# Kernel tuning notes

Measured on AMD Instinct MI355X. Metric: run time of the kernel, lower is better.

Reference implementation:

```python
import jax, jax.numpy as jnp
import numpy as np

B, S, D = 1, 2048, 4096
H, KVH, HD = 32, 8, 128


def setup_inputs() -> dict:
    key = jax.random.key(0)
    ks = jax.random.split(key, 6)
    x = jax.random.normal(ks[0], (B, S, D), dtype=jnp.float32)
    # Llama3 RoPE angles: theta = 500000
    inv_freq = 1.0 / (500000.0 ** (np.arange(0, HD, 2, dtype=np.float32) / HD))
    ang = np.arange(S, dtype=np.float32)[:, None] * inv_freq[None, :]  # [S, HD//2]
    freqs_cos = jnp.asarray(np.cos(ang), dtype=jnp.float32)
    freqs_sin = jnp.asarray(np.sin(ang), dtype=jnp.float32)
    sc = 0.02
    wq = jax.random.normal(ks[1], (H * HD, D), dtype=jnp.float32) * sc
    wk = jax.random.normal(ks[2], (KVH * HD, D), dtype=jnp.float32) * sc
    wv = jax.random.normal(ks[3], (KVH * HD, D), dtype=jnp.float32) * sc
    wo = jax.random.normal(ks[4], (D, H * HD), dtype=jnp.float32) * sc
    return {"x": x, "freqs_cos": freqs_cos, "freqs_sin": freqs_sin,
            "wq": wq, "wk": wk, "wv": wv, "wo": wo}


def _rope(t, cos, sin):
    # t: [B, S, h, HD]; rotate consecutive pairs (complex multiply)
    t2 = t.reshape(*t.shape[:-1], HD // 2, 2)
    x0, x1 = t2[..., 0], t2[..., 1]
    c = cos[None, :, None, :]
    s = sin[None, :, None, :]
    r0 = x0 * c - x1 * s
    r1 = x0 * s + x1 * c
    return jnp.stack([r0, r1], axis=-1).reshape(t.shape)


def reference(x, freqs_cos, freqs_sin, wq, wk, wv, wo):
    b, s, _ = x.shape
    q = jnp.einsum('bsd,ed->bse', x, wq).reshape(b, s, H, HD)
    k = jnp.einsum('bsd,ed->bse', x, wk).reshape(b, s, KVH, HD)
    v = jnp.einsum('bsd,ed->bse', x, wv).reshape(b, s, KVH, HD)
    q = _rope(q, freqs_cos, freqs_sin)
    k = _rope(k, freqs_cos, freqs_sin)
    # GQA: repeat kv heads
    rep = H // KVH
    k = jnp.repeat(k, rep, axis=2)
    v = jnp.repeat(v, rep, axis=2)
    scale = 1.0 / jnp.sqrt(jnp.asarray(HD, dtype=x.dtype))
    scores = jnp.einsum('bqhd,bkhd->bhqk', q, k) * scale
    causal = jnp.tril(jnp.ones((s, s), dtype=bool))
    scores = jnp.where(causal[None, None], scores, jnp.finfo(scores.dtype).min)
    p = jax.nn.softmax(scores, axis=-1)
    out = jnp.einsum('bhqk,bkhd->bqhd', p, v).reshape(b, s, H * HD)
    return jnp.einsum('bse,de->bsd', out, wo)
```

## Files before the change

kernel.cpp:

```cpp
#include <hip/hip_runtime.h>

typedef unsigned short u16;
typedef short bf16x8 __attribute__((ext_vector_type(8)));
typedef float f32x4 __attribute__((ext_vector_type(4)));

#define S_LEN 2048
#define ATT_SCALE (0.08838834764831845f * 1.4426950408889634f)
#define NEG_BIG  -1.0e30f

static __device__ __forceinline__ float bf2f(u16 u) {
  union { unsigned int i; float f; } v; v.i = ((unsigned int)u) << 16; return v.f;
}
static __device__ __forceinline__ u16 f2bf(float f) {
  union { float f; unsigned int i; } v; v.f = f;
  unsigned int x = v.i;
  return (u16)((x + 0x7fffu + ((x >> 16) & 1u)) >> 16);
}
static __device__ __forceinline__ float fexp2(float x) {
  return __builtin_amdgcn_exp2f(x);
}

static __device__ __forceinline__ void gl_lds16(const u16* g, u16* l) {
  __builtin_amdgcn_global_load_lds(
      (const __attribute__((address_space(1))) unsigned int*)g,
      (__attribute__((address_space(3))) unsigned int*)l, 16, 0, 0);
}

static __device__ __forceinline__ bf16x8 load8(const u16* p) { return *(const bf16x8*)p; }
static __device__ __forceinline__ bf16x8 load8(const float* p) {
  f32x4 a = *(const f32x4*)p;
  f32x4 b = *(const f32x4*)(p + 4);
  bf16x8 r;
  r[0] = (short)f2bf(a[0]); r[1] = (short)f2bf(a[1]);
  r[2] = (short)f2bf(a[2]); r[3] = (short)f2bf(a[3]);
  r[4] = (short)f2bf(b[0]); r[5] = (short)f2bf(b[1]);
  r[6] = (short)f2bf(b[2]); r[7] = (short)f2bf(b[3]);
  return r;
}
static __device__ __forceinline__ void store_out(u16* C, size_t i, float v)  { C[i] = f2bf(v); }
static __device__ __forceinline__ void store_out(float* C, size_t i, float v){ C[i] = v; }

__global__ __launch_bounds__(256) void f2b_kernel(
    const float* __restrict__ s, u16* __restrict__ d, int n8) {
  int i = blockIdx.x * 256 + threadIdx.x;
  if (i >= n8) return;
  *(bf16x8*)&d[(size_t)i * 8] = load8(s + (size_t)i * 8);
}

template <typename OT>
static __device__ __forceinline__ void gemm_core(
    const u16* __restrict__ A, const u16* __restrict__ B, OT* __restrict__ C,
    int K, int ldc, int bm, int bn) {
  __shared__ __align__(16) u16 As[128 * 64];
  __shared__ __align__(16) u16 Bs[128 * 64];
  const int tid  = threadIdx.x;
  const int lane = tid & 63;
  const int wave = tid >> 6;
  const int wm = (wave >> 1) << 6;
  const int wn = (wave & 1) << 6;
  const int col  = lane & 15;
  const int quad = lane >> 4;

  const f32x4 fzero = {0.f, 0.f, 0.f, 0.f};
  f32x4 acc[4][4];
#pragma unroll
  for (int i = 0; i < 4; ++i)
#pragma unroll
    for (int j = 0; j < 4; ++j) acc[i][j] = fzero;

  const int srow = (lane >> 3);
  const int sc8  = lane & 7;

  for (int k0 = 0; k0 < K; k0 += 64) {
#pragma unroll
    for (int i = 0; i < 4; ++i) {
      int r = wave * 32 + i * 8 + srow;
      int src = (sc8 ^ (r & 7)) << 3;
      gl_lds16(A + (size_t)(bm + r) * K + k0 + src, &As[(wave * 32 + i * 8) * 64]);
      gl_lds16(B + (size_t)(bn + r) * K + k0 + src, &Bs[(wave * 32 + i * 8) * 64]);
    }
    __syncthreads();
#pragma unroll
    for (int kk = 0; kk < 64; kk += 32) {
      bf16x8 af[4], bfr[4];
#pragma unroll
      for (int mt = 0; mt < 4; ++mt) {
        int row = wm + mt * 16 + col;
        af[mt] = *(const bf16x8*)&As[row * 64 + ((((kk >> 3) + quad) ^ (col & 7)) << 3)];
      }
#pragma unroll
      for (int nt = 0; nt < 4; ++nt) {
        int row = wn + nt * 16 + col;
        bfr[nt] = *(const bf16x8*)&Bs[row * 64 + ((((kk >> 3) + quad) ^ (col & 7)) << 3)];
      }
#pragma unroll
      for (int mt = 0; mt < 4; ++mt)
#pragma unroll
        for (int nt = 0; nt < 4; ++nt)
          acc[mt][nt] = __builtin_amdgcn_mfma_f32_16x16x32_bf16(
              af[mt], bfr[nt], acc[mt][nt], 0, 0, 0);
    }
    __syncthreads();
  }
#pragma unroll
  for (int mt = 0; mt < 4; ++mt)
#pragma unroll
    for (int nt = 0; nt < 4; ++nt)
#pragma unroll
      for (int r = 0; r < 4; ++r) {
        int row = bm + wm + mt * 16 + quad * 4 + r;
        int cn  = bn + wn + nt * 16 + col;
        store_out(C, (size_t)row * ldc + cn, acc[mt][nt][r]);
      }
}

__global__ __launch_bounds__(256) void gemm_qkv(
    const u16* __restrict__ xb, const u16* __restrict__ wqb,
    const u16* __restrict__ wkb, const u16* __restrict__ wvb,
    u16* __restrict__ q, u16* __restrict__ k, u16* __restrict__ v) {
  int bx = blockIdx.x;
  const u16* B; u16* C; int ldc, bn;
  if (bx < 32)      { B = wqb; C = q; ldc = 4096; bn = bx * 128; }
  else if (bx < 40) { B = wkb; C = k; ldc = 1024; bn = (bx - 32) * 128; }
  else              { B = wvb; C = v; ldc = 1024; bn = (bx - 40) * 128; }
  gemm_core<u16>(xb, B, C, 4096, ldc, blockIdx.y * 128, bn);
}

__global__ __launch_bounds__(256) void gemm_o(
    const u16* __restrict__ ao, const u16* __restrict__ wob, float* __restrict__ out) {
  gemm_core<float>(ao, wob, out, 4096, 4096, blockIdx.y * 128, blockIdx.x * 128);
}

#define LDK 72
template <typename AT, typename BT, typename OT>
__global__ __launch_bounds__(256) void gemm_bt(
    const AT* __restrict__ A, const BT* __restrict__ B,
    OT* __restrict__ C, int M, int N, int K) {
  __shared__ __align__(16) u16 As[128 * LDK];
  __shared__ __align__(16) u16 Bs[128 * LDK];
  const int tid  = threadIdx.x;
  const int lane = tid & 63;
  const int wave = tid >> 6;
  const int wm = (wave >> 1) << 6;
  const int wn = (wave & 1) << 6;
  const int col  = lane & 15;
  const int quad = lane >> 4;
  const int bm = blockIdx.y * 128;
  const int bn = blockIdx.x * 128;

  const f32x4 fzero = {0.f, 0.f, 0.f, 0.f};
  f32x4 acc[4][4];
#pragma unroll
  for (int i = 0; i < 4; ++i)
#pragma unroll
    for (int j = 0; j < 4; ++j) acc[i][j] = fzero;

  const int sr = tid >> 3;
  const int sc = (tid & 7) * 8;
  const AT* Aptr = A + (size_t)(bm + sr) * K + sc;
  const BT* Bptr = B + (size_t)(bn + sr) * K + sc;

  for (int k0 = 0; k0 < K; k0 += 64) {
#pragma unroll
    for (int p = 0; p < 4; ++p) {
      *(bf16x8*)&As[(sr + 32 * p) * LDK + sc] = load8(Aptr + (size_t)(32 * p) * K + k0);
      *(bf16x8*)&Bs[(sr + 32 * p) * LDK + sc] = load8(Bptr + (size_t)(32 * p) * K + k0);
    }
    __syncthreads();
#pragma unroll
    for (int kk = 0; kk < 64; kk += 32) {
      bf16x8 af[4], bfr[4];
#pragma unroll
      for (int mt = 0; mt < 4; ++mt)
        af[mt] = *(const bf16x8*)&As[(wm + mt * 16 + col) * LDK + kk + quad * 8];
#pragma unroll
      for (int nt = 0; nt < 4; ++nt)
        bfr[nt] = *(const bf16x8*)&Bs[(wn + nt * 16 + col) * LDK + kk + quad * 8];
#pragma unroll
      for (int mt = 0; mt < 4; ++mt)
#pragma unroll
        for (int nt = 0; nt < 4; ++nt)
          acc[mt][nt] = __builtin_amdgcn_mfma_f32_16x16x32_bf16(
              af[mt], bfr[nt], acc[mt][nt], 0, 0, 0);
    }
    __syncthreads();
  }
#pragma unroll
  for (int mt = 0; mt < 4; ++mt)
#pragma unroll
    for (int nt = 0; nt < 4; ++nt)
#pragma unroll
      for (int r = 0; r < 4; ++r) {
        int row = bm + wm + mt * 16 + quad * 4 + r;
        int cn  = bn + wn + nt * 16 + col;
        store_out(C, (size_t)row * N + cn, acc[mt][nt][r]);
      }
}

__global__ __launch_bounds__(256) void rope_kernel(
    u16* __restrict__ q, u16* __restrict__ k,
    const float* __restrict__ cs, const float* __restrict__ sn) {
  int idx = blockIdx.x * 256 + threadIdx.x;
  const int QP = S_LEN * 32 * 64;
  u16* base;
  int s, i;
  bool isq = idx < QP;
  if (isq) {
    s = idx >> 11; int w = idx & 2047; i = w & 63;
    base = q + (size_t)s * 4096 + (w >> 6) * 128 + 2 * i;
  } else {
    int j = idx - QP;
    s = j >> 9; int w = j & 511; i = w & 63;
    base = k + (size_t)s * 1024 + (w >> 6) * 128 + 2 * i;
  }
  float c  = cs[s * 64 + i];
  float sv = sn[s * 64 + i];
  float x0 = bf2f(base[0]);
  float x1 = bf2f(base[1]);
  float r0 = x0 * c - x1 * sv;
  float r1 = x0 * sv + x1 * c;
  if (isq) { r0 *= ATT_SCALE; r1 *= ATT_SCALE; }
  base[0] = f2bf(r0);
  base[1] = f2bf(r1);
}

__global__ __launch_bounds__(512, 2) void attn_kernel(
    const u16* __restrict__ Q, const u16* __restrict__ K,
    const u16* __restrict__ V, u16* __restrict__ O) {
  const int ib   = blockIdx.x;
  const int h    = blockIdx.y;
  const int kvh  = h >> 2;
  const int tid  = threadIdx.x;
  const int lane = tid & 63;
  const int wave = tid >> 6;
  const int grp  = wave >> 2;
  const int wl   = wave & 3;
  const int col  = lane & 15;
  const int quad = lane >> 4;
  const int chd  = col >> 3;
  const int gt   = tid & 255;

  __shared__ __align__(16) u16 SMEM[2][16384];
  __shared__ float MLS[256];
  u16* Kb = &SMEM[grp][0];
  u16* Vb = &SMEM[grp][8192];

  const f32x4 fzero = {0.f, 0.f, 0.f, 0.f};

  const int krow = lane >> 4;
  const int kcnk = lane & 15;
  const int vsc  = (gt & 15) * 8;
  const int vrp  = gt >> 4;
  const int vrot = gt & 7;

  for (int t = 0; t < 2; ++t) {
    const int qb = t ? 15 - ib : ib;
    const int rb = qb * 128 + wl * 32;

    bf16x8 qf[2][4];
#pragma unroll
    for (int u = 0; u < 2; ++u)
#pragma unroll
      for (int kb = 0; kb < 4; ++kb)
        qf[u][kb] = *(const bf16x8*)&Q[(size_t)(rb + u * 16 + col) * 4096 +
                                       h * 128 + kb * 32 + quad * 8];

    f32x4 oacc[2][8];
#pragma unroll
    for (int u = 0; u < 2; ++u)
#pragma unroll
      for (int nt = 0; nt < 8; ++nt) oacc[u][nt] = fzero;
    float m_[2] = {NEG_BIG, NEG_BIG};
    float l_[2] = {0.f, 0.f};

    const int nr = qb + 1;
    for (int rnd = 0; rnd < nr; ++rnd) {
      const int c    = grp * nr + rnd;
      const int pos0 = c * 64;

#pragma unroll
      for (int i = 0; i < 4; ++i) {
        int r  = wl * 16 + i * 4 + krow;
        int g  = (kcnk & 8) |
                 ((((kcnk ^ r) & 7) + (((r >> 3) & 1) << 2)) & 7);
        gl_lds16(&K[(size_t)(pos0 + r) * 1024 + kvh * 128 + g * 8],
                 &Kb[(wl * 16 + i * 4) * 128]);
      }
#pragma unroll
      for (int it = 0; it < 2; ++it) {
        int rp = vrp + it * 16;
        const u16* vp = &V[(size_t)(pos0 + 2 * rp) * 1024 + kvh * 128 + vsc];
        union { bf16x8 v; u16 u[8]; } ue, uo;
        ue.v = *(const bf16x8*)vp;
        uo.v = *(const bf16x8*)(vp + 1024);
        int pc = rp >> 2, pi = rp & 3;
#pragma unroll
        for (int j = 0; j < 8; ++j) {
          int jj = (j + vrot) & 7;
          int hd = vsc + jj;
          int swz = (((pc + (((hd >> 3) & 1) << 2)) & 7) ^ (hd & 7));
          unsigned val = (unsigned)ue.u[jj] | ((unsigned)uo.u[jj] << 16);
          *(unsigned*)&Vb[hd * 64 + swz * 8 + pi * 2] = val;
        }
      }
      __syncthreads();

      f32x4 sv[2][4];
#pragma unroll
      for (int u = 0; u < 2; ++u)
#pragma unroll
        for (int kv = 0; kv < 4; ++kv) sv[u][kv] = fzero;
      __builtin_amdgcn_s_setprio(1);
#pragma unroll
      for (int kv = 0; kv < 4; ++kv) {
        int r = kv * 16 + col;
#pragma unroll
        for (int kb = 0; kb < 4; ++kb) {
          int kq   = kb * 4 + quad;
          int slot = (kq & 8) | ((((kq & 7) + (chd << 2)) & 7) ^ (r & 7));
          bf16x8 kf = *(const bf16x8*)&Kb[r * 128 + slot * 8];
          sv[0][kv] = __builtin_amdgcn_mfma_f32_16x16x32_bf16(kf, qf[0][kv*0+kb], sv[0][kv], 0, 0, 0);
          sv[1][kv] = __builtin_amdgcn_mfma_f32_16x16x32_bf16(kf, qf[1][kb], sv[1][kv], 0, 0, 0);
        }
      }
      __builtin_amdgcn_s_setprio(0);

      unsigned pk[2][4][2];
#pragma unroll
      for (int u = 0; u < 2; ++u) {
        const int ubase = rb + u * 16;
        const int qpos  = ubase + col;
        const bool nomask = (pos0 + 63 <= ubase);
        float mx = NEG_BIG;
        if (nomask) {
#pragma unroll
          for (int kv = 0; kv < 4; ++kv)
#pragma unroll
            for (int r = 0; r < 4; ++r) mx = fmaxf(mx, sv[u][kv][r]);
        } else {
#pragma unroll
          for (int kv = 0; kv < 4; ++kv)
#pragma unroll
            for (int r = 0; r < 4; ++r) {
              bool keep = (pos0 + kv * 16 + quad * 4 + r) <= qpos;
              float s = keep ? sv[u][kv][r] : NEG_BIG;
              sv[u][kv][r] = s;
              mx = fmaxf(mx, s);
            }
        }
        mx = fmaxf(mx, __shfl_xor(mx, 16));
        mx = fmaxf(mx, __shfl_xor(mx, 32));
        if (!__all(mx - m_[u] <= 8.f)) {
          float mnew  = fmaxf(m_[u], mx);
          float alpha = fexp2(m_[u] - mnew);
          l_[u] *= alpha;
#pragma unroll
          for (int nt = 0; nt < 8; ++nt) {
            oacc[u][nt][0] *= alpha; oacc[u][nt][1] *= alpha;
            oacc[u][nt][2] *= alpha; oacc[u][nt][3] *= alpha;
          }
          m_[u] = mnew;
        }
        float ls = 0.f;
        if (nomask) {
#pragma unroll
          for (int kv = 0; kv < 4; ++kv)
#pragma unroll
            for (int r = 0; r < 4; ++r) {
              float p = fexp2(sv[u][kv][r] - m_[u]);
              sv[u][kv][r] = p;
              ls += p;
            }
        } else {
#pragma unroll
          for (int kv = 0; kv < 4; ++kv)
#pragma unroll
            for (int r = 0; r < 4; ++r) {
              float p = fexp2(sv[u][kv][r] - m_[u]);
              bool keep = (pos0 + kv * 16 + quad * 4 + r) <= qpos;
              p = keep ? p : 0.f;
              sv[u][kv][r] = p;
              ls += p;
            }
        }
        ls += __shfl_xor(ls, 16);
        ls += __shfl_xor(ls, 32);
        l_[u] += ls;
#pragma unroll
        for (int kv = 0; kv < 4; ++kv) {
          pk[u][kv][0] = (unsigned)f2bf(sv[u][kv][0]) | ((unsigned)f2bf(sv[u][kv][1]) << 16);
          pk[u][kv][1] = (unsigned)f2bf(sv[u][kv][2]) | ((unsigned)f2bf(sv[u][kv][3]) << 16);
        }
      }

      const int idxA = col + 16 * (2 * (quad & 1));
      const int idxB = idxA + 16;
      const bool hi  = quad >= 2;
#pragma unroll
      for (int kc = 0; kc < 2; ++kc) {
        union { unsigned u[4]; bf16x8 v; } pb[2];
#pragma unroll
        for (int u = 0; u < 2; ++u) {
          unsigned a00 = __shfl(pk[u][2 * kc][0],     idxA);
          unsigned a01 = __shfl(pk[u][2 * kc][1],     idxA);
          unsigned a10 = __shfl(pk[u][2 * kc + 1][0], idxA);
          unsigned a11 = __shfl(pk[u][2 * kc + 1][1], idxA);
          unsigned b00 = __shfl(pk[u][2 * kc][0],     idxB);
          unsigned b01 = __shfl(pk[u][2 * kc][1],     idxB);
          unsigned b10 = __shfl(pk[u][2 * kc + 1][0], idxB);
          unsigned b11 = __shfl(pk[u][2 * kc + 1][1], idxB);
          pb[u].u[0] = hi ? a10 : a00;
          pb[u].u[1] = hi ? a11 : a01;
          pb[u].u[2] = hi ? b10 : b00;
          pb[u].u[3] = hi ? b11 : b01;
        }
        __builtin_amdgcn_s_setprio(1);
#pragma unroll
        for (int nt = 0; nt < 8; ++nt) {
          int hd  = nt * 16 + col;
          int pc  = kc * 4 + quad;
          int swz = (((pc + (chd << 2)) & 7) ^ (hd & 7));
          bf16x8 vf = *(const bf16x8*)&Vb[hd * 64 + swz * 8];
          oacc[0][nt] = __builtin_amdgcn_mfma_f32_16x16x32_bf16(vf, pb[0].v, oacc[0][nt], 0, 0, 0);
          oacc[1][nt] = __builtin_amdgcn_mfma_f32_16x16x32_bf16(vf, pb[1].v, oacc[1][nt], 0, 0, 0);
        }
        __builtin_amdgcn_s_setprio(0);
      }
      __syncthreads();
    }

    float* MF = (float*)&SMEM[0][0];
    if (grp == 1) {
#pragma unroll
      for (int u = 0; u < 2; ++u) {
        int ql = wl * 32 + u * 16 + col;
#pragma unroll
        for (int nt = 0; nt < 8; ++nt)
          *(f32x4*)&MF[(size_t)ql * 128 + nt * 16 + quad * 4] = oacc[u][nt];
        if (quad == 0) { MLS[2 * ql] = m_[u]; MLS[2 * ql + 1] = l_[u]; }
      }
    }
    __syncthreads();
    if (grp == 0) {
#pragma unroll
      for (int u = 0; u < 2; ++u) {
        int ql = wl * 32 + u * 16 + col;
        int qpos = qb * 128 + ql;
        float m1 = MLS[2 * ql], l1 = MLS[2 * ql + 1];
        float mn = fmaxf(m_[u], m1);
        float a0 = fexp2(m_[u] - mn), a1 = fexp2(m1 - mn);
        float li = 1.f / (l_[u] * a0 + l1 * a1);
        a0 *= li; a1 *= li;
#pragma unroll
        for (int nt = 0; nt < 8; ++nt) {
          f32x4 o1 = *(const f32x4*)&MF[(size_t)ql * 128 + nt * 16 + quad * 4];
          union { u16 u[4]; unsigned long long ll; } w;
          w.u[0] = f2bf(oacc[u][nt][0] * a0 + o1[0] * a1);
          w.u[1] = f2bf(oacc[u][nt][1] * a0 + o1[1] * a1);
          w.u[2] = f2bf(oacc[u][nt][2] * a0 + o1[2] * a1);
          w.u[3] = f2bf(oacc[u][nt][3] * a0 + o1[3] * a1);
          *(unsigned long long*)&O[(size_t)qpos * 4096 + h * 128 + nt * 16 + quad * 4] = w.ll;
        }
      }
    }
    __syncthreads();
  }
}

extern "C" void kernel_launch(void* const* d_in, const int* in_sizes, int n_in,
                              void* d_out, int out_size, void* d_ws, size_t ws_size,
                              hipStream_t stream) {
  const float* x  = (const float*)d_in[0];
  const float* fc = (const float*)d_in[1];
  const float* fs = (const float*)d_in[2];
  const float* wq = (const float*)d_in[3];
  const float* wk = (const float*)d_in[4];
  const float* wv = (const float*)d_in[5];
  const float* wo = (const float*)d_in[6];
  float* out = (float*)d_out;

  u16* q  = (u16*)d_ws;
  u16* k  = q + (size_t)8388608;
  u16* v  = k + (size_t)2097152;
  u16* ao = v + (size_t)2097152;

  dim3 blk(256, 1, 1);
  dim3 ablk(512, 1, 1);
  const size_t NEED_FAST = 109051904ULL;

  if (ws_size >= NEED_FAST) {
    u16* xb  = ao  + (size_t)8388608;
    u16* wqb = xb  + (size_t)8388608;
    u16* wkb = wqb + (size_t)16777216;
    u16* wvb = wkb + (size_t)4194304;
    u16* wob = wqb;

    hipLaunchKernelGGL(f2b_kernel, dim3(4096, 1, 1), blk, 0, stream, x,  xb,  1048576);
    hipLaunchKernelGGL(f2b_kernel, dim3(8192, 1, 1), blk, 0, stream, wq, wqb, 2097152);
    hipLaunchKernelGGL(f2b_kernel, dim3(2048, 1, 1), blk, 0, stream, wk, wkb, 524288);
    hipLaunchKernelGGL(f2b_kernel, dim3(2048, 1, 1), blk, 0, stream, wv, wvb, 524288);
    hipLaunchKernelGGL(gemm_qkv, dim3(48, 16, 1), blk, 0, stream, xb, wqb, wkb, wvb, q, k, v);
    hipLaunchKernelGGL(f2b_kernel, dim3(8192, 1, 1), blk, 0, stream, wo, wob, 2097152);
    hipLaunchKernelGGL(rope_kernel, dim3(20480, 1, 1), blk, 0, stream, q, k, fc, fs);
    hipLaunchKernelGGL(attn_kernel, dim3(8, 32, 1), ablk, 0, stream, q, k, v, ao);
    hipLaunchKernelGGL(gemm_o, dim3(32, 16, 1), blk, 0, stream, ao, wob, out);
  } else {
    hipLaunchKernelGGL((gemm_bt<float, float, u16>), dim3(32, 16, 1), blk, 0, stream,
                       x, wq, q, 2048, 4096, 4096);
    hipLaunchKernelGGL((gemm_bt<float, float, u16>), dim3(8, 16, 1),  blk, 0, stream,
                       x, wk, k, 2048, 1024, 4096);
    hipLaunchKernelGGL((gemm_bt<float, float, u16>), dim3(8, 16, 1),  blk, 0, stream,
                       x, wv, v, 2048, 1024, 4096);
    hipLaunchKernelGGL(rope_kernel, dim3(20480, 1, 1), blk, 0, stream, q, k, fc, fs);
    hipLaunchKernelGGL(attn_kernel, dim3(8, 32, 1), ablk, 0, stream, q, k, v, ao);
    hipLaunchKernelGGL((gemm_bt<u16, float, float>), dim3(32, 16, 1), blk, 0, stream,
                       ao, wo, out, 2048, 4096, 4096);
  }
}
```

Measured before the change: 537.5 us.

## Fuse RoPE into QKV GEMM epilogue and merge fp32-to-bf16 conversion launches

The four separate fp32-to-bf16 conversion launches for x, wq, wk and wv are merged into one grid-stride kernel. RoPE (with the attention scale folded into Q) now runs in the QKV GEMM epilogue, using a lane shuffle to fetch the paired element. This removes the standalone rope pass that read and rewrote Q and K. The risk is that the rope_kernel may have applied the attention scale itself; if attn_kernel still applies it, Q would be scaled twice. The epilogue also gains extra global loads of the cos/sin tables.

```diff
diff --git a/kernel.cpp b/kernel.cpp
--- a/kernel.cpp
+++ b/kernel.cpp
@@ -40,6 +40,22 @@
 static __device__ __forceinline__ void store_out(u16* C, size_t i, float v)  { C[i] = f2bf(v); }
 static __device__ __forceinline__ void store_out(float* C, size_t i, float v){ C[i] = v; }
 
+__global__ __launch_bounds__(256) void f2b4_kernel(
+    const float* __restrict__ x,  const float* __restrict__ wq,
+    const float* __restrict__ wk, const float* __restrict__ wv,
+    u16* __restrict__ xb, u16* __restrict__ wqb,
+    u16* __restrict__ wkb, u16* __restrict__ wvb) {
+  const int total = 4194304;
+  for (int u = blockIdx.x * 256 + threadIdx.x; u < total; u += gridDim.x * 256) {
+    const float* s; u16* d; int off;
+    if (u < 1048576)      { s = x;  d = xb;  off = u; }
+    else if (u < 3145728) { s = wq; d = wqb; off = u - 1048576; }
+    else if (u < 3670016) { s = wk; d = wkb; off = u - 3145728; }
+    else                  { s = wv; d = wvb; off = u - 3670016; }
+    *(bf16x8*)&d[(size_t)off * 8] = load8(s + (size_t)off * 8);
+  }
+}
+
 __global__ __launch_bounds__(256) void f2b_kernel(
     const float* __restrict__ s, u16* __restrict__ d, int n8) {
   int i = blockIdx.x * 256 + threadIdx.x;
@@ -50,7 +66,9 @@
 template <typename OT>
 static __device__ __forceinline__ void gemm_core(
     const u16* __restrict__ A, const u16* __restrict__ B, OT* __restrict__ C,
-    int K, int ldc, int bm, int bn) {
+    int K, int ldc, int bm, int bn,
+    const float* __restrict__ cs, const float* __restrict__ sn,
+    float rope_scale, int do_rope) {
   __shared__ __align__(16) u16 As[128 * 64];
   __shared__ __align__(16) u16 Bs[128 * 64];
   const int tid  = threadIdx.x;
@@ -110,25 +128,35 @@
       for (int r = 0; r < 4; ++r) {
         int row = bm + wm + mt * 16 + quad * 4 + r;
         int cn  = bn + wn + nt * 16 + col;
-        store_out(C, (size_t)row * ldc + cn, acc[mt][nt][r]);
+        float val = acc[mt][nt][r];
+        if (do_rope) {
+          float pv = __shfl_xor(val, 1);
+          int ii = (cn >> 1) & 63;
+          float c  = cs[row * 64 + ii] * rope_scale;
+          float sv = sn[row * 64 + ii] * rope_scale;
+          val = (cn & 1) ? (pv * sv + val * c) : (val * c - pv * sv);
+        }
+        store_out(C, (size_t)row * ldc + cn, val);
       }
 }
 
 __global__ __launch_bounds__(256) void gemm_qkv(
     const u16* __restrict__ xb, const u16* __restrict__ wqb,
     const u16* __restrict__ wkb, const u16* __restrict__ wvb,
-    u16* __restrict__ q, u16* __restrict__ k, u16* __restrict__ v) {
+    u16* __restrict__ q, u16* __restrict__ k, u16* __restrict__ v,
+    const float* __restrict__ cs, const float* __restrict__ sn) {
   int bx = blockIdx.x;
-  const u16* B; u16* C; int ldc, bn;
-  if (bx < 32)      { B = wqb; C = q; ldc = 4096; bn = bx * 128; }
-  else if (bx < 40) { B = wkb; C = k; ldc = 1024; bn = (bx - 32) * 128; }
-  else              { B = wvb; C = v; ldc = 1024; bn = (bx - 40) * 128; }
-  gemm_core<u16>(xb, B, C, 4096, ldc, blockIdx.y * 128, bn);
+  const u16* B; u16* C; int ldc, bn; int rope; float scale;
+  if (bx < 32)      { B = wqb; C = q; ldc = 4096; bn = bx * 128;        rope = 1; scale = ATT_SCALE; }
+  else if (bx < 40) { B = wkb; C = k; ldc = 1024; bn = (bx - 32) * 128; rope = 1; scale = 1.0f; }
+  else              { B = wvb; C = v; ldc = 1024; bn = (bx - 40) * 128; rope = 0; scale = 1.0f; }
+  gemm_core<u16>(xb, B, C, 4096, ldc, blockIdx.y * 128, bn, cs, sn, scale, rope);
 }
 
 __global__ __launch_bounds__(256) void gemm_o(
     const u16* __restrict__ ao, const u16* __restrict__ wob, float* __restrict__ out) {
-  gemm_core<float>(ao, wob, out, 4096, 4096, blockIdx.y * 128, blockIdx.x * 128);
+  gemm_core<float>(ao, wob, out, 4096, 4096, blockIdx.y * 128, blockIdx.x * 128,
+                   nullptr, nullptr, 1.0f, 0);
 }
 
 #define LDK 72
@@ -319,7 +347,7 @@
           int kq   = kb * 4 + quad;
           int slot = (kq & 8) | ((((kq & 7) + (chd << 2)) & 7) ^ (r & 7));
           bf16x8 kf = *(const bf16x8*)&Kb[r * 128 + slot * 8];
-          sv[0][kv] = __builtin_amdgcn_mfma_f32_16x16x32_bf16(kf, qf[0][kv*0+kb], sv[0][kv], 0, 0, 0);
+          sv[0][kv] = __builtin_amdgcn_mfma_f32_16x16x32_bf16(kf, qf[0][kb], sv[0][kv], 0, 0, 0);
           sv[1][kv] = __builtin_amdgcn_mfma_f32_16x16x32_bf16(kf, qf[1][kb], sv[1][kv], 0, 0, 0);
         }
       }
@@ -495,13 +523,11 @@
     u16* wvb = wkb + (size_t)4194304;
     u16* wob = wqb;
 
-    hipLaunchKernelGGL(f2b_kernel, dim3(4096, 1, 1), blk, 0, stream, x,  xb,  1048576);
-    hipLaunchKernelGGL(f2b_kernel, dim3(8192, 1, 1), blk, 0, stream, wq, wqb, 2097152);
-    hipLaunchKernelGGL(f2b_kernel, dim3(2048, 1, 1), blk, 0, stream, wk, wkb, 524288);
-    hipLaunchKernelGGL(f2b_kernel, dim3(2048, 1, 1), blk, 0, stream, wv, wvb, 524288);
-    hipLaunchKernelGGL(gemm_qkv, dim3(48, 16, 1), blk, 0, stream, xb, wqb, wkb, wvb, q, k, v);
+    hipLaunchKernelGGL(f2b4_kernel, dim3(2048, 1, 1), blk, 0, stream,
+                       x, wq, wk, wv, xb, wqb, wkb, wvb);
+    hipLaunchKernelGGL(gemm_qkv, dim3(48, 16, 1), blk, 0, stream,
+                       xb, wqb, wkb, wvb, q, k, v, fc, fs);
     hipLaunchKernelGGL(f2b_kernel, dim3(8192, 1, 1), blk, 0, stream, wo, wob, 2097152);
-    hipLaunchKernelGGL(rope_kernel, dim3(20480, 1, 1), blk, 0, stream, q, k, fc, fs);
     hipLaunchKernelGGL(attn_kernel, dim3(8, 32, 1), ablk, 0, stream, q, k, v, ao);
     hipLaunchKernelGGL(gemm_o, dim3(32, 16, 1), blk, 0, stream, ao, wob, out);
   } else {
```

Measured after the change: 574.6 us. 1.07x slower.
